# Kernel tuning notes

Hardware: AMD Instinct MI355X
Metric: run time of the kernel (lower is better)

Reference implementation:

```python
import jax, jax.numpy as jnp
import numpy as np

N = 8192   # num_neurons
P = 64     # num stored patterns


def setup_inputs() -> dict:
    key = jax.random.key(0)
    k1, k2 = jax.random.split(key)
    # Bipolar (+/-1) stored patterns, as in classical Hopfield usage
    X = jnp.where(jax.random.normal(k1, (N, P)) >= 0, 1.0, -1.0).astype(jnp.float32)
    # Initial (possibly corrupted) bipolar state
    state = jnp.where(jax.random.normal(k2, (N,)) >= 0, 1.0, -1.0).astype(jnp.float32)
    # Visit order for asynchronous updates (torch.randperm in original; any permutation is valid)
    perm = jnp.arange(N, dtype=jnp.int32)
    return {"X": X, "state": state, "perm": perm}


def reference(X, state, perm):
    n = X.shape[0]
    # W = X X^T / N with zero diagonal (Hebbian weights), as in __init__
    W = (X @ X.T) / n                                  # [N, N]
    W = W * (1.0 - jnp.eye(n, dtype=W.dtype))
    # Strictly sequential asynchronous update over the given permutation
    def step(s, i):
        act = jnp.dot(W[i], s)                         # dot(W[i], new_state)
        s = s.at[i].set(jnp.where(act >= 0, 1.0, -1.0).astype(s.dtype))
        return s, None
    final_state, _ = jax.lax.scan(step, state, perm)
    return final_state
```

## Files before the change

### kernel.cpp

```cpp
#include <hip/hip_runtime.h>
#include <stdint.h>


#define NB 128
typedef unsigned long long u64;
typedef unsigned u32;


__global__ __launch_bounds__(256) void hop_prep(
    const float* __restrict__ X, const float* __restrict__ state,
    const int* __restrict__ perm, float* __restrict__ m0,
    float* __restrict__ Yt, u64* __restrict__ sig, u64* __restrict__ sigT,
    float* __restrict__ sps)
{
  const int b = blockIdx.x, t = threadIdx.x;
  const int wv = t >> 6, ln = t & 63;
  __shared__ u64 sigL[64];
  __shared__ float red[4][64];

  float acc = 0.f;
  #pragma unroll
  for (int jj = 0; jj < 16; ++jj) {
    const int j = wv*16 + jj;
    const int r = perm[b*64 + j];
    const float sr = state[r];
    const float x = X[(size_t)r*64 + ln];
    Yt[(size_t)b*4096 + (ln >> 2)*256 + j*4 + (ln & 3)] = x * sr;
    u64 bb = __ballot(x < 0.f);
    if (sr < 0.f) bb = ~bb;
    if (ln == 0) { sig[b*64 + j] = bb; sigL[j] = bb; }
    acc = fmaf(x, sr, acc);
  }
  red[wv][ln] = acc;
  __syncthreads();

  {
    const u64 gs = sigL[ln];
    #pragma unroll
    for (int jj = 0; jj < 16; ++jj) {
      const int p = wv*16 + jj;
      u64 tb = __ballot((unsigned)((gs >> p) & 1ull));
      if (ln == 0) sigT[b*64 + p] = tb;
    }
  }

  if (t < 64) {
    atomicAdd(&m0[t], (red[0][t] + red[1][t]) + (red[2][t] + red[3][t]));
    sps[b*64 + t] = state[perm[b*64 + t]];
  }
}

#define PROCESS(Y, gsig, gsigT, rr, ss) {                                     \
  float q0=0.f,q1=0.f,q2=0.f,q3=0.f;                                          \
  const float4* mv4 = (const float4*)mlds;                                    \
  _Pragma("unroll")                                                           \
  for (int g = 0; g < 16; ++g) {                                              \
    const float4 yv = Y[g]; const float4 mv = mv4[g];                         \
    q0 = fmaf(yv.x, mv.x, q0); q1 = fmaf(yv.y, mv.y, q1);                     \
    q2 = fmaf(yv.z, mv.z, q2); q3 = fmaf(yv.w, mv.w, q3);                     \
  }                                                                           \
  const float qf = (q0+q1)+(q2+q3);                 \
  int T = ((int)qf << 1) - (((ss) < 0.f) ? 1 : 0);                            \
  u64 flips;                                                                  \
  {                                                                           \
    const u32 siglo = (u32)(gsig), sighi = (u32)((gsig) >> 32);               \
    int thr = 128;                                                            \
    u64 live, mm, bit; u32 i_, t0, t1, v0, v1;                                \
    asm volatile(                                                             \
      "s_mov_b64 %[flips], 0\n\t"                                             \
      "s_mov_b64 %[live], -1\n\t"                                             \
      "1:\n\t"                                                                \
      "v_cmp_gt_i32 vcc, %[thr], %[T]\n\t"                     \
      "s_and_b64 %[mm], vcc, %[live]\n\t"                       \
      "s_cbranch_scc0 2f\n\t"                                                 \
      "s_ff1_i32_b64 %[i], %[mm]\n\t"                                         \
      "v_readlane_b32 %[t0], %[siglo], %[i]\n\t"                              \
      "v_readlane_b32 %[t1], %[sighi], %[i]\n\t"                              \
      "s_lshl_b64 %[bit], 1, %[i]\n\t"               \
      "s_or_b64 %[flips], %[flips], %[bit]\n\t"      \
      "s_lshl_b64 %[live], -2, %[i]\n\t"             \
      "s_addk_i32 %[thr], 0x100\n\t"                          \
      "v_xor_b32 %[v0], %[t0], %[siglo]\n\t"                                  \
      "v_xor_b32 %[v1], %[t1], %[sighi]\n\t"                                  \
      "v_bcnt_u32_b32 %[v0], %[v0], 0\n\t"                                    \
      "v_bcnt_u32_b32 %[v0], %[v1], %[v0]\n\t"                                \
      "v_lshl_add_u32 %[T], %[v0], 3, %[T]\n\t"              \
      "s_branch 1b\n\t"                                                       \
      "2:\n\t"                                                                \
      : [flips]"=&s"(flips), [live]"=&s"(live), [mm]"=&s"(mm),                \
        [bit]"=&s"(bit), [i]"=&s"(i_), [t0]"=&s"(t0), [t1]"=&s"(t1),          \
        [thr]"+s"(thr), [T]"+v"(T), [v0]"=&v"(v0), [v1]"=&v"(v1)              \
      : [siglo]"v"(siglo), [sighi]"v"(sighi)                                  \
      : "vcc", "scc");                                                        \
  }                                                                           \
  if (flips) {                                                                \
    const int nf = (int)__popcll(flips);                                      \
    const int pc = (int)__popcll(flips & (gsigT));                            \
    mreg += (float)(4*pc - 2*nf);                                             \
    mlds[lane] = mreg;                                                        \
  }                                                                           \
  out[rr] = ((flips >> lane) & 1ull) ? -(ss) : (ss);                          \
}

__global__ __launch_bounds__(64) void hop_solve(
    const int* __restrict__ perm, const float* __restrict__ m0,
    const float4* __restrict__ Yt4, const u64* __restrict__ sig,
    const u64* __restrict__ sigT, const float* __restrict__ sps,
    float* __restrict__ out)
{
  __shared__ __align__(16) float mlds[64];
  const int lane = threadIdx.x;

  float mreg = m0[lane];
  mlds[lane] = mreg;

  float4 Ya[16], Yb[16];
  u64 sgA, stA, sgB, stB; int rA, rB; float sA, sB;

  {
    const float4* yp = Yt4 + lane;
    #pragma unroll
    for (int g = 0; g < 16; ++g) Ya[g] = yp[g*64];
    sgA = sig[lane]; stA = sigT[lane]; rA = perm[lane]; sA = sps[lane];
  }

  for (int bb = 0; bb < NB; bb += 2) {
    {
      const int bn = bb + 1;
      const float4* yp = Yt4 + (size_t)bn*1024 + lane;
      #pragma unroll
      for (int g = 0; g < 16; ++g) Yb[g] = yp[g*64];
      sgB = sig[bn*64+lane]; stB = sigT[bn*64+lane];
      rB = perm[bn*64+lane]; sB = sps[bn*64+lane];
    }
    PROCESS(Ya, sgA, stA, rA, sA);
    {
      const int bn = (bb + 2 < NB) ? bb + 2 : NB - 1;
      const float4* yp = Yt4 + (size_t)bn*1024 + lane;
      #pragma unroll
      for (int g = 0; g < 16; ++g) Ya[g] = yp[g*64];
      sgA = sig[bn*64+lane]; stA = sigT[bn*64+lane];
      rA = perm[bn*64+lane]; sA = sps[bn*64+lane];
    }
    PROCESS(Yb, sgB, stB, rB, sB);
  }
}

extern "C" void kernel_launch(void* const* d_in, const int* in_sizes, int n_in,
                              void* d_out, int out_size, void* d_ws, size_t ws_size,
                              hipStream_t stream) {
  const float* X     = (const float*)d_in[0];
  const float* state = (const float*)d_in[1];
  const int*   perm  = (const int*)d_in[2];
  float* outp = (float*)d_out;

  float* m0  = (float*)d_ws;
  float* Yt  = m0 + 64;
  u64*   sig = (u64*)(Yt + 128*4096);
  u64*   sigT= sig + 8192;
  float* sps = (float*)(sigT + 8192);

  hipMemsetAsync(m0, 0, 64*sizeof(float), stream);
  hop_prep<<<dim3(NB), dim3(256), 0, stream>>>(X, state, perm, m0, Yt, sig, sigT, sps);
  hop_solve<<<dim3(1), dim3(64), 0, stream>>>(perm, m0, (const float4*)Yt, sig, sigT, sps, outp);
}
```

Before: 368.2 us.

## Stage Y blocks via global_load_lds into swizzled LDS and unroll flip scan

```diff
diff --git a/kernel.cpp b/kernel.cpp
--- a/kernel.cpp
+++ b/kernel.cpp
@@ -7,10 +7,16 @@
 typedef unsigned u32;
 
 
+__device__ __forceinline__ void glds16(const void* g, void* l) {
+  __builtin_amdgcn_global_load_lds(
+      (const __attribute__((address_space(1))) void*)g,
+      (__attribute__((address_space(3))) void*)l, 16, 0, 0);
+}
+
 __global__ __launch_bounds__(256) void hop_prep(
     const float* __restrict__ X, const float* __restrict__ state,
     const int* __restrict__ perm, float* __restrict__ m0,
-    float* __restrict__ Yt, u64* __restrict__ sig, u64* __restrict__ sigT,
+    float* __restrict__ Ysw, u64* __restrict__ sig, u64* __restrict__ sigT,
     float* __restrict__ sps)
 {
   const int b = blockIdx.x, t = threadIdx.x;
@@ -25,7 +31,7 @@
     const int r = perm[b*64 + j];
     const float sr = state[r];
     const float x = X[(size_t)r*64 + ln];
-    Yt[(size_t)b*4096 + (ln >> 2)*256 + j*4 + (ln & 3)] = x * sr;
+    Ysw[(size_t)b*4096 + j*64 + ((((ln >> 2) ^ (j & 7)) << 2) | (ln & 3))] = x * sr;
     u64 bb = __ballot(x < 0.f);
     if (sr < 0.f) bb = ~bb;
     if (ln == 0) { sig[b*64 + j] = bb; sigL[j] = bb; }
@@ -50,99 +56,157 @@
   }
 }
 
-#define PROCESS(Y, gsig, gsigT, rr, ss) {                                     \
-  float q0=0.f,q1=0.f,q2=0.f,q3=0.f;                                          \
-  const float4* mv4 = (const float4*)mlds;                                    \
-  _Pragma("unroll")                                                           \
-  for (int g = 0; g < 16; ++g) {                                              \
-    const float4 yv = Y[g]; const float4 mv = mv4[g];                         \
-    q0 = fmaf(yv.x, mv.x, q0); q1 = fmaf(yv.y, mv.y, q1);                     \
-    q2 = fmaf(yv.z, mv.z, q2); q3 = fmaf(yv.w, mv.w, q3);                     \
-  }                                                                           \
-  const float qf = (q0+q1)+(q2+q3);                 \
-  int T = ((int)qf << 1) - (((ss) < 0.f) ? 1 : 0);                            \
-  u64 flips;                                                                  \
-  {                                                                           \
-    const u32 siglo = (u32)(gsig), sighi = (u32)((gsig) >> 32);               \
-    int thr = 128;                                                            \
-    u64 live, mm, bit; u32 i_, t0, t1, v0, v1;                                \
-    asm volatile(                                                             \
-      "s_mov_b64 %[flips], 0\n\t"                                             \
-      "s_mov_b64 %[live], -1\n\t"                                             \
-      "1:\n\t"                                                                \
-      "v_cmp_gt_i32 vcc, %[thr], %[T]\n\t"                     \
-      "s_and_b64 %[mm], vcc, %[live]\n\t"                       \
-      "s_cbranch_scc0 2f\n\t"                                                 \
-      "s_ff1_i32_b64 %[i], %[mm]\n\t"                                         \
-      "v_readlane_b32 %[t0], %[siglo], %[i]\n\t"                              \
-      "v_readlane_b32 %[t1], %[sighi], %[i]\n\t"                              \
-      "s_lshl_b64 %[bit], 1, %[i]\n\t"               \
-      "s_or_b64 %[flips], %[flips], %[bit]\n\t"      \
-      "s_lshl_b64 %[live], -2, %[i]\n\t"             \
-      "s_addk_i32 %[thr], 0x100\n\t"                          \
-      "v_xor_b32 %[v0], %[t0], %[siglo]\n\t"                                  \
-      "v_xor_b32 %[v1], %[t1], %[sighi]\n\t"                                  \
-      "v_bcnt_u32_b32 %[v0], %[v0], 0\n\t"                                    \
-      "v_bcnt_u32_b32 %[v0], %[v1], %[v0]\n\t"                                \
-      "v_lshl_add_u32 %[T], %[v0], 3, %[T]\n\t"              \
-      "s_branch 1b\n\t"                                                       \
-      "2:\n\t"                                                                \
-      : [flips]"=&s"(flips), [live]"=&s"(live), [mm]"=&s"(mm),                \
-        [bit]"=&s"(bit), [i]"=&s"(i_), [t0]"=&s"(t0), [t1]"=&s"(t1),          \
-        [thr]"+s"(thr), [T]"+v"(T), [v0]"=&v"(v0), [v1]"=&v"(v1)              \
-      : [siglo]"v"(siglo), [sighi]"v"(sighi)                                  \
-      : "vcc", "scc");                                                        \
-  }                                                                           \
-  if (flips) {                                                                \
-    const int nf = (int)__popcll(flips);                                      \
-    const int pc = (int)__popcll(flips & (gsigT));                            \
-    mreg += (float)(4*pc - 2*nf);                                             \
-    mlds[lane] = mreg;                                                        \
-  }                                                                           \
-  out[rr] = ((flips >> lane) & 1ull) ? -(ss) : (ss);                          \
-}
+#define CORE(I, B, FH) \
+  "v_cmp_gt_i32 vcc, %[thr], %[T]\n\t" \
+  "v_lshl_add_u32 %[Ts], %[c], 3, %[T]\n\t" \
+  "s_bitcmp1_b64 vcc, " I "\n\t" \
+  "s_cselect_b64 %[msk], -1, 0\n\t" \
+  "s_cselect_b32 %[bt], " B ", 0\n\t" \
+  "s_cselect_b32 %[inc], 0x100, 0\n\t" \
+  "s_or_b32 %[" FH "], %[" FH "], %[bt]\n\t" \
+  "s_add_i32 %[thr], %[thr], %[inc]\n\t" \
+  "v_cndmask_b32 %[T], %[T], %[Ts], %[msk]\n\t"
+
+#define SF(I, IN, B, FH) \
+  "v_readlane_b32 %[t0], %[slo], " IN "\n\t" \
+  "v_readlane_b32 %[t1], %[shi], " IN "\n\t" \
+  CORE(I, B, FH) \
+  "v_xor_b32 %[x0], %[t0], %[slo]\n\t" \
+  "v_xor_b32 %[x1], %[t1], %[shi]\n\t" \
+  "v_bcnt_u32_b32 %[c], %[x0], 0\n\t" \
+  "v_bcnt_u32_b32 %[c], %[x1], %[c]\n\t"
+
+#define GENT0(FIRST) \
+  "v_cmp_gt_i32 vcc, %[thr], %[T]\n\t" \
+  "v_readlane_b32 %[t0], %[slo], " FIRST "\n\t" \
+  "v_readlane_b32 %[t1], %[shi], " FIRST "\n\t" \
+  "s_cmp_lg_u64 vcc, 0\n\t" \
+  "s_cbranch_scc0 7f\n\t" \
+  "v_xor_b32 %[x0], %[t0], %[slo]\n\t" \
+  "v_xor_b32 %[x1], %[t1], %[shi]\n\t" \
+  "v_bcnt_u32_b32 %[c], %[x0], 0\n\t" \
+  "v_bcnt_u32_b32 %[c], %[x1], %[c]\n\t"
+
+#define GENT(FIRST, SHIFT) \
+  "v_cmp_gt_i32 vcc, %[thr], %[T]\n\t" \
+  "v_readlane_b32 %[t0], %[slo], " FIRST "\n\t" \
+  "v_readlane_b32 %[t1], %[shi], " FIRST "\n\t" \
+  "s_lshr_b64 %[msk], vcc, " SHIFT "\n\t" \
+  "s_cmp_lg_u64 %[msk], 0\n\t" \
+  "s_cbranch_scc0 7f\n\t" \
+  "v_xor_b32 %[x0], %[t0], %[slo]\n\t" \
+  "v_xor_b32 %[x1], %[t1], %[shi]\n\t" \
+  "v_bcnt_u32_b32 %[c], %[x0], 0\n\t" \
+  "v_bcnt_u32_b32 %[c], %[x1], %[c]\n\t"
 
 __global__ __launch_bounds__(64) void hop_solve(
     const int* __restrict__ perm, const float* __restrict__ m0,
-    const float4* __restrict__ Yt4, const u64* __restrict__ sig,
+    const float* __restrict__ Ysw, const u64* __restrict__ sig,
     const u64* __restrict__ sigT, const float* __restrict__ sps,
     float* __restrict__ out)
 {
   __shared__ __align__(16) float mlds[64];
+  __shared__ __align__(16) float Ybuf[2][4096];
   const int lane = threadIdx.x;
 
   float mreg = m0[lane];
   mlds[lane] = mreg;
 
-  float4 Ya[16], Yb[16];
-  u64 sgA, stA, sgB, stB; int rA, rB; float sA, sB;
-
   {
-    const float4* yp = Yt4 + lane;
+    const float* ys = Ysw + lane*4;
     #pragma unroll
-    for (int g = 0; g < 16; ++g) Ya[g] = yp[g*64];
-    sgA = sig[lane]; stA = sigT[lane]; rA = perm[lane]; sA = sps[lane];
-  }
-
-  for (int bb = 0; bb < NB; bb += 2) {
-    {
-      const int bn = bb + 1;
-      const float4* yp = Yt4 + (size_t)bn*1024 + lane;
+    for (int it = 0; it < 16; ++it) glds16(ys + it*256, &Ybuf[0][it*256]);
+  }
+  u64 sgA = sig[lane], stA = sigT[lane];
+  int rA = perm[lane]; float sA = sps[lane];
+  asm volatile("s_waitcnt vmcnt(0)" ::: "memory");
+
+  int cur = 0;
+  for (int b = 0; b < NB; ++b) {
+    u64 sgB = 0, stB = 0; int rB = 0; float sB = 0.f;
+    if (b + 1 < NB) {
+      const float* ys = Ysw + (size_t)(b+1)*4096 + lane*4;
       #pragma unroll
-      for (int g = 0; g < 16; ++g) Yb[g] = yp[g*64];
-      sgB = sig[bn*64+lane]; stB = sigT[bn*64+lane];
-      rB = perm[bn*64+lane]; sB = sps[bn*64+lane];
-    }
-    PROCESS(Ya, sgA, stA, rA, sA);
-    {
-      const int bn = (bb + 2 < NB) ? bb + 2 : NB - 1;
-      const float4* yp = Yt4 + (size_t)bn*1024 + lane;
-      #pragma unroll
-      for (int g = 0; g < 16; ++g) Ya[g] = yp[g*64];
-      sgA = sig[bn*64+lane]; stA = sigT[bn*64+lane];
-      rA = perm[bn*64+lane]; sA = sps[bn*64+lane];
-    }
-    PROCESS(Yb, sgB, stB, rB, sB);
+      for (int it = 0; it < 16; ++it) glds16(ys + it*256, &Ybuf[cur^1][it*256]);
+      sgB = sig[(b+1)*64+lane]; stB = sigT[(b+1)*64+lane];
+      rB = perm[(b+1)*64+lane]; sB = sps[(b+1)*64+lane];
+    }
+
+    const float* Yc = Ybuf[cur];
+    float q0=0.f,q1=0.f,q2=0.f,q3=0.f;
+    const float4* mv4 = (const float4*)mlds;
+    #pragma unroll
+    for (int g = 0; g < 16; ++g) {
+      const float4 yv = *(const float4*)&Yc[lane*64 + ((g ^ (lane & 7)) << 2)];
+      const float4 mv = mv4[g];
+      q0 = fmaf(yv.x, mv.x, q0); q1 = fmaf(yv.y, mv.y, q1);
+      q2 = fmaf(yv.z, mv.z, q2); q3 = fmaf(yv.w, mv.w, q3);
+    }
+    int T = ((int)((q0+q1)+(q2+q3)) << 1) - ((sA < 0.f) ? 1 : 0);
+
+    const u32 slo = (u32)sgA, shi = (u32)(sgA >> 32);
+    u32 flo = 0, fhi = 0; int thr = 128;
+    u32 t0, t1, x0, x1, c, bt, inc; int Ts; u64 msk;
+    asm volatile(
+      GENT0("0")
+      SF("0","1","1","flo") SF("1","2","2","flo") SF("2","3","4","flo")
+      SF("3","4","8","flo") SF("4","5","0x10","flo") SF("5","6","0x20","flo")
+      SF("6","7","0x40","flo") SF("7","8","0x80","flo") SF("8","9","0x100","flo")
+      SF("9","10","0x200","flo") SF("10","11","0x400","flo")
+      SF("11","12","0x800","flo") SF("12","13","0x1000","flo")
+      SF("13","14","0x2000","flo") SF("14","15","0x4000","flo")
+      CORE("15","0x8000","flo")
+      "7:\n\t"
+      GENT("16","16")
+      SF("16","17","0x10000","flo") SF("17","18","0x20000","flo")
+      SF("18","19","0x40000","flo") SF("19","20","0x80000","flo")
+      SF("20","21","0x100000","flo") SF("21","22","0x200000","flo")
+      SF("22","23","0x400000","flo") SF("23","24","0x800000","flo")
+      SF("24","25","0x1000000","flo") SF("25","26","0x2000000","flo")
+      SF("26","27","0x4000000","flo") SF("27","28","0x8000000","flo")
+      SF("28","29","0x10000000","flo") SF("29","30","0x20000000","flo")
+      SF("30","31","0x40000000","flo")
+      CORE("31","0x80000000","flo")
+      "7:\n\t"
+      GENT("32","32")
+      SF("32","33","1","fhi") SF("33","34","2","fhi") SF("34","35","4","fhi")
+      SF("35","36","8","fhi") SF("36","37","0x10","fhi") SF("37","38","0x20","fhi")
+      SF("38","39","0x40","fhi") SF("39","40","0x80","fhi")
+      SF("40","41","0x100","fhi") SF("41","42","0x200","fhi")
+      SF("42","43","0x400","fhi") SF("43","44","0x800","fhi")
+      SF("44","45","0x1000","fhi") SF("45","46","0x2000","fhi")
+      SF("46","47","0x4000","fhi")
+      CORE("47","0x8000","fhi")
+      "7:\n\t"
+      GENT("48","48")
+      SF("48","49","0x10000","fhi") SF("49","50","0x20000","fhi")
+      SF("50","51","0x40000","fhi") SF("51","52","0x80000","fhi")
+      SF("52","53","0x100000","fhi") SF("53","54","0x200000","fhi")
+      SF("54","55","0x400000","fhi") SF("55","56","0x800000","fhi")
+      SF("56","57","0x1000000","fhi") SF("57","58","0x2000000","fhi")
+      SF("58","59","0x4000000","fhi") SF("59","60","0x8000000","fhi")
+      SF("60","61","0x10000000","fhi") SF("61","62","0x20000000","fhi")
+      SF("62","63","0x40000000","fhi")
+      CORE("63","0x80000000","fhi")
+      "7:\n\t"
+      : [T]"+v"(T), [thr]"+s"(thr), [flo]"+s"(flo), [fhi]"+s"(fhi),
+        [t0]"=&s"(t0), [t1]"=&s"(t1), [x0]"=&v"(x0), [x1]"=&v"(x1),
+        [c]"=&v"(c), [Ts]"=&v"(Ts), [msk]"=&s"(msk), [bt]"=&s"(bt),
+        [inc]"=&s"(inc)
+      : [slo]"v"(slo), [shi]"v"(shi)
+      : "vcc", "scc");
+
+    const u64 flips = ((u64)fhi << 32) | (u64)flo;
+    if (flips) {
+      const int nf = (int)__popcll(flips);
+      const int pc = (int)__popcll(flips & stA);
+      mreg += (float)(4*pc - 2*nf);
+      mlds[lane] = mreg;
+    }
+    out[rA] = ((flips >> lane) & 1ull) ? -sA : sA;
+
+    asm volatile("s_waitcnt vmcnt(1)" ::: "memory");
+    sgA = sgB; stA = stB; rA = rB; sA = sB; cur ^= 1;
   }
 }
 
@@ -155,12 +219,12 @@
   float* outp = (float*)d_out;
 
   float* m0  = (float*)d_ws;
-  float* Yt  = m0 + 64;
-  u64*   sig = (u64*)(Yt + 128*4096);
+  float* Ysw = m0 + 64;
+  u64*   sig = (u64*)(Ysw + 128*4096);
   u64*   sigT= sig + 8192;
   float* sps = (float*)(sigT + 8192);
 
   hipMemsetAsync(m0, 0, 64*sizeof(float), stream);
-  hop_prep<<<dim3(NB), dim3(256), 0, stream>>>(X, state, perm, m0, Yt, sig, sigT, sps);
-  hop_solve<<<dim3(1), dim3(64), 0, stream>>>(perm, m0, (const float4*)Yt, sig, sigT, sps, outp);
-}
+  hop_prep<<<dim3(NB), dim3(256), 0, stream>>>(X, state, perm, m0, Ysw, sig, sigT, sps);
+  hop_solve<<<dim3(1), dim3(64), 0, stream>>>(perm, m0, Ysw, sig, sigT, sps, outp);
+}
```

New measurement: 482.3 us. 31.0% more time.

## Stage Y blocks through swizzled LDS via direct global-to-LDS loads and unroll flip loop

Applied to the files above, without the earlier changes.

```diff
diff --git a/kernel.cpp b/kernel.cpp
--- a/kernel.cpp
+++ b/kernel.cpp
@@ -7,10 +7,16 @@
 typedef unsigned u32;
 
 
+__device__ __forceinline__ void glds16(const void* g, void* l) {
+  __builtin_amdgcn_global_load_lds(
+      (const __attribute__((address_space(1))) void*)g,
+      (__attribute__((address_space(3))) void*)l, 16, 0, 0);
+}
+
 __global__ __launch_bounds__(256) void hop_prep(
     const float* __restrict__ X, const float* __restrict__ state,
     const int* __restrict__ perm, float* __restrict__ m0,
-    float* __restrict__ Yt, u64* __restrict__ sig, u64* __restrict__ sigT,
+    float* __restrict__ Ysw, u64* __restrict__ sig, u64* __restrict__ sigT,
     float* __restrict__ sps)
 {
   const int b = blockIdx.x, t = threadIdx.x;
@@ -25,7 +31,7 @@
     const int r = perm[b*64 + j];
     const float sr = state[r];
     const float x = X[(size_t)r*64 + ln];
-    Yt[(size_t)b*4096 + (ln >> 2)*256 + j*4 + (ln & 3)] = x * sr;
+    Ysw[(size_t)b*4096 + j*64 + ((((ln >> 2) ^ (j & 7)) << 2) | (ln & 3))] = x * sr;
     u64 bb = __ballot(x < 0.f);
     if (sr < 0.f) bb = ~bb;
     if (ln == 0) { sig[b*64 + j] = bb; sigL[j] = bb; }
@@ -50,99 +56,99 @@
   }
 }
 
-#define PROCESS(Y, gsig, gsigT, rr, ss) {                                     \
+#define STEP \
+  "s_ff1_i32_b64 %[i], %[mm]\n\t" \
+  "v_readlane_b32 %[t0], %[slo], %[i]\n\t" \
+  "v_readlane_b32 %[t1], %[shi], %[i]\n\t" \
+  "s_lshl_b64 %[bit], 1, %[i]\n\t" \
+  "s_or_b64 %[flips], %[flips], %[bit]\n\t" \
+  "s_lshl_b64 %[live], -2, %[i]\n\t" \
+  "s_addk_i32 %[thr], 0x100\n\t" \
+  "v_xor_b32 %[x0], %[t0], %[slo]\n\t" \
+  "v_xor_b32 %[x1], %[t1], %[shi]\n\t" \
+  "v_bcnt_u32_b32 %[c], %[x0], 0\n\t" \
+  "v_bcnt_u32_b32 %[c], %[x1], %[c]\n\t" \
+  "v_lshl_add_u32 %[T], %[c], 3, %[T]\n\t" \
+  "v_cmp_gt_i32 vcc, %[thr], %[T]\n\t" \
+  "s_and_b64 %[mm], vcc, %[live]\n\t"
+
+#define PROCESS(YB, sg, st, rr, ss) {                                         \
+  const float* Yc = (YB);                                                     \
   float q0=0.f,q1=0.f,q2=0.f,q3=0.f;                                          \
   const float4* mv4 = (const float4*)mlds;                                    \
   _Pragma("unroll")                                                           \
   for (int g = 0; g < 16; ++g) {                                              \
-    const float4 yv = Y[g]; const float4 mv = mv4[g];                         \
+    const float4 yv = *(const float4*)&Yc[ybase + ((g ^ lswz) << 2)];         \
+    const float4 mv = mv4[g];                                                 \
     q0 = fmaf(yv.x, mv.x, q0); q1 = fmaf(yv.y, mv.y, q1);                     \
     q2 = fmaf(yv.z, mv.z, q2); q3 = fmaf(yv.w, mv.w, q3);                     \
   }                                                                           \
-  const float qf = (q0+q1)+(q2+q3);                 \
-  int T = ((int)qf << 1) - (((ss) < 0.f) ? 1 : 0);                            \
-  u64 flips;                                                                  \
+  int T = ((int)((q0+q1)+(q2+q3)) << 1) - (((ss) < 0.f) ? 1 : 0);             \
+  const u32 slo = (u32)(sg), shi = (u32)((sg) >> 32);                         \
+  u64 flips; int thr = 128;                                                   \
   {                                                                           \
-    const u32 siglo = (u32)(gsig), sighi = (u32)((gsig) >> 32);               \
-    int thr = 128;                                                            \
-    u64 live, mm, bit; u32 i_, t0, t1, v0, v1;                                \
+    u64 live, mm, bit; u32 i_, t0, t1, x0, x1, c;                             \
     asm volatile(                                                             \
       "s_mov_b64 %[flips], 0\n\t"                                             \
       "s_mov_b64 %[live], -1\n\t"                                             \
+      "v_cmp_gt_i32 vcc, %[thr], %[T]\n\t"                                    \
+      "s_and_b64 %[mm], vcc, %[live]\n\t"                                     \
+      "s_cbranch_scc0 9f\n\t"                                                 \
       "1:\n\t"                                                                \
-      "v_cmp_gt_i32 vcc, %[thr], %[T]\n\t"                     \
-      "s_and_b64 %[mm], vcc, %[live]\n\t"                       \
-      "s_cbranch_scc0 2f\n\t"                                                 \
-      "s_ff1_i32_b64 %[i], %[mm]\n\t"                                         \
-      "v_readlane_b32 %[t0], %[siglo], %[i]\n\t"                              \
-      "v_readlane_b32 %[t1], %[sighi], %[i]\n\t"                              \
-      "s_lshl_b64 %[bit], 1, %[i]\n\t"               \
-      "s_or_b64 %[flips], %[flips], %[bit]\n\t"      \
-      "s_lshl_b64 %[live], -2, %[i]\n\t"             \
-      "s_addk_i32 %[thr], 0x100\n\t"                          \
-      "v_xor_b32 %[v0], %[t0], %[siglo]\n\t"                                  \
-      "v_xor_b32 %[v1], %[t1], %[sighi]\n\t"                                  \
-      "v_bcnt_u32_b32 %[v0], %[v0], 0\n\t"                                    \
-      "v_bcnt_u32_b32 %[v0], %[v1], %[v0]\n\t"                                \
-      "v_lshl_add_u32 %[T], %[v0], 3, %[T]\n\t"              \
-      "s_branch 1b\n\t"                                                       \
-      "2:\n\t"                                                                \
+      STEP "s_cbranch_scc0 9f\n\t"                                            \
+      STEP "s_cbranch_scc0 9f\n\t"                                            \
+      STEP "s_cbranch_scc0 9f\n\t"                                            \
+      STEP "s_cbranch_scc1 1b\n\t"                                            \
+      "9:\n\t"                                                                \
       : [flips]"=&s"(flips), [live]"=&s"(live), [mm]"=&s"(mm),                \
         [bit]"=&s"(bit), [i]"=&s"(i_), [t0]"=&s"(t0), [t1]"=&s"(t1),          \
-        [thr]"+s"(thr), [T]"+v"(T), [v0]"=&v"(v0), [v1]"=&v"(v1)              \
-      : [siglo]"v"(siglo), [sighi]"v"(sighi)                                  \
+        [thr]"+s"(thr), [T]"+v"(T), [x0]"=&v"(x0), [x1]"=&v"(x1),             \
+        [c]"=&v"(c)                                                           \
+      : [slo]"v"(slo), [shi]"v"(shi)                                          \
       : "vcc", "scc");                                                        \
   }                                                                           \
-  if (flips) {                                                                \
+  if (flips) {        \
     const int nf = (int)__popcll(flips);                                      \
-    const int pc = (int)__popcll(flips & (gsigT));                            \
+    const int pc = (int)__popcll(flips & (st));                               \
     mreg += (float)(4*pc - 2*nf);                                             \
     mlds[lane] = mreg;                                                        \
   }                                                                           \
   out[rr] = ((flips >> lane) & 1ull) ? -(ss) : (ss);                          \
 }
 
+#define PREFETCH(BN, BUF, sg, st, rr, ss) {                                   \
+  const float* ys = Ysw + (size_t)(BN)*4096 + lane*4;                         \
+  _Pragma("unroll")                                                           \
+  for (int it = 0; it < 16; ++it) glds16(ys + it*256, &(BUF)[it*256]);        \
+  sg = sig[(BN)*64+lane]; st = sigT[(BN)*64+lane];                            \
+  rr = perm[(BN)*64+lane]; ss = sps[(BN)*64+lane];                            \
+}
+
 __global__ __launch_bounds__(64) void hop_solve(
     const int* __restrict__ perm, const float* __restrict__ m0,
-    const float4* __restrict__ Yt4, const u64* __restrict__ sig,
+    const float* __restrict__ Ysw, const u64* __restrict__ sig,
     const u64* __restrict__ sigT, const float* __restrict__ sps,
     float* __restrict__ out)
 {
   __shared__ __align__(16) float mlds[64];
+  __shared__ __align__(16) float Ybuf[2][4096];
   const int lane = threadIdx.x;
+  const int ybase = lane*64, lswz = lane & 7;
 
   float mreg = m0[lane];
   mlds[lane] = mreg;
 
-  float4 Ya[16], Yb[16];
   u64 sgA, stA, sgB, stB; int rA, rB; float sA, sB;
-
-  {
-    const float4* yp = Yt4 + lane;
-    #pragma unroll
-    for (int g = 0; g < 16; ++g) Ya[g] = yp[g*64];
-    sgA = sig[lane]; stA = sigT[lane]; rA = perm[lane]; sA = sps[lane];
-  }
+  PREFETCH(0, Ybuf[0], sgA, stA, rA, sA);
+  asm volatile("s_waitcnt vmcnt(0)" ::: "memory");
 
   for (int bb = 0; bb < NB; bb += 2) {
-    {
-      const int bn = bb + 1;
-      const float4* yp = Yt4 + (size_t)bn*1024 + lane;
-      #pragma unroll
-      for (int g = 0; g < 16; ++g) Yb[g] = yp[g*64];
-      sgB = sig[bn*64+lane]; stB = sigT[bn*64+lane];
-      rB = perm[bn*64+lane]; sB = sps[bn*64+lane];
-    }
-    PROCESS(Ya, sgA, stA, rA, sA);
-    {
-      const int bn = (bb + 2 < NB) ? bb + 2 : NB - 1;
-      const float4* yp = Yt4 + (size_t)bn*1024 + lane;
-      #pragma unroll
-      for (int g = 0; g < 16; ++g) Ya[g] = yp[g*64];
-      sgA = sig[bn*64+lane]; stA = sigT[bn*64+lane];
-      rA = perm[bn*64+lane]; sA = sps[bn*64+lane];
-    }
-    PROCESS(Yb, sgB, stB, rB, sB);
+    PREFETCH(bb+1, Ybuf[1], sgB, stB, rB, sB);
+    PROCESS(Ybuf[0], sgA, stA, rA, sA);
+    asm volatile("s_waitcnt vmcnt(1)" ::: "memory");
+    if (bb + 2 < NB) PREFETCH(bb+2, Ybuf[0], sgA, stA, rA, sA);
+    PROCESS(Ybuf[1], sgB, stB, rB, sB);
+    asm volatile("s_waitcnt vmcnt(1)" ::: "memory");
   }
 }
 
@@ -155,12 +161,12 @@
   float* outp = (float*)d_out;
 
   float* m0  = (float*)d_ws;
-  float* Yt  = m0 + 64;
-  u64*   sig = (u64*)(Yt + 128*4096);
+  float* Ysw = m0 + 64;
+  u64*   sig = (u64*)(Ysw + 128*4096);
   u64*   sigT= sig + 8192;
   float* sps = (float*)(sigT + 8192);
 
   hipMemsetAsync(m0, 0, 64*sizeof(float), stream);
-  hop_prep<<<dim3(NB), dim3(256), 0, stream>>>(X, state, perm, m0, Yt, sig, sigT, sps);
-  hop_solve<<<dim3(1), dim3(64), 0, stream>>>(perm, m0, (const float4*)Yt, sig, sigT, sps, outp);
+  hop_prep<<<dim3(NB), dim3(256), 0, stream>>>(X, state, perm, m0, Ysw, sig, sigT, sps);
+  hop_solve<<<dim3(1), dim3(64), 0, stream>>>(perm, m0, Ysw, sig, sigT, sps, outp);
 }
```

Measured after the change: 389.6 us. 1.06x slower.
